# Kernel tuning notes

Hardware: AMD Instinct MI355X
Metric: run time of the kernel (lower is better)

## Reference

```python
import jax, jax.numpy as jnp
import numpy as np

B = 128      # graphs in batch
NPG = 128    # nodes per graph
F = 256      # num_node_features
D = 192      # d_model
NH = 8       # decoder heads
L = 4        # decoder layers
DFF = 512
DEG = 16     # avg degree
P = 32       # num_patch_nodes
EH = 96      # encoder_hidden = max(D//2, 48)
GH = 4       # GAT heads (layer 1)
EPS = 1e-5


def _init(key, shape, fan_in):
    return jax.random.normal(key, shape, jnp.float32) / np.sqrt(fan_in)


def setup_inputs() -> dict:
    key = jax.random.key(0)
    ks = jax.random.split(key, 40)
    N = B * NPG
    E = N * DEG
    off = jnp.repeat(jnp.arange(B, dtype=jnp.int32) * NPG, E // B)
    src = jax.random.randint(ks[1], (E,), 0, NPG, dtype=jnp.int32) + off
    dst = jax.random.randint(ks[2], (E,), 0, NPG, dtype=jnp.int32) + off
    inp = dict(
        subgraph_x=jax.random.normal(ks[0], (N, F), jnp.float32),
        subgraph_edge_index=jnp.stack([src, dst]),
        target_local_idx=jax.random.randint(ks[3], (B,), 0, NPG, dtype=jnp.int32),
        batch=jnp.repeat(jnp.arange(B, dtype=jnp.int32), NPG),
        num_patch_nodes=P,
    )
    # GAT encoder params (PyG GATConv layout: W [heads*out, in], att [heads, out])
    inp['gat1_w'] = _init(ks[4], (GH * EH, F), F)
    inp['gat1_att_src'] = _init(ks[5], (GH, EH), EH)
    inp['gat1_att_dst'] = _init(ks[6], (GH, EH), EH)
    inp['gat1_b'] = jnp.zeros((GH * EH,), jnp.float32)
    inp['gat2_w'] = _init(ks[7], (D, GH * EH), GH * EH)
    inp['gat2_att_src'] = _init(ks[8], (1, D), D)
    inp['gat2_att_dst'] = _init(ks[9], (1, D), D)
    inp['gat2_b'] = jnp.zeros((D,), jnp.float32)
    # TransformerDecoder layers (stacked over L)
    inp['sa_qkv_w'] = _init(ks[10], (L, 3 * D, D), D)
    inp['sa_qkv_b'] = jnp.zeros((L, 3 * D), jnp.float32)
    inp['sa_out_w'] = _init(ks[11], (L, D, D), D)
    inp['sa_out_b'] = jnp.zeros((L, D), jnp.float32)
    inp['ca_qkv_w'] = _init(ks[12], (L, 3 * D, D), D)
    inp['ca_qkv_b'] = jnp.zeros((L, 3 * D), jnp.float32)
    inp['ca_out_w'] = _init(ks[13], (L, D, D), D)
    inp['ca_out_b'] = jnp.zeros((L, D), jnp.float32)
    inp['ff1_w'] = _init(ks[14], (L, DFF, D), D)
    inp['ff1_b'] = jnp.zeros((L, DFF), jnp.float32)
    inp['ff2_w'] = _init(ks[15], (L, D, DFF), DFF)
    inp['ff2_b'] = jnp.zeros((L, D), jnp.float32)
    inp['ln_g'] = jnp.ones((L, 3, D), jnp.float32)
    inp['ln_b'] = jnp.zeros((L, 3, D), jnp.float32)
    # feature head
    inp['h1_w'] = _init(ks[16], (D, D), D)
    inp['h1_b'] = jnp.zeros((D,), jnp.float32)
    inp['h2_w'] = _init(ks[17], (F, D), D)
    inp['h2_b'] = jnp.zeros((F,), jnp.float32)
    return inp


def _gat(x, src, dst, W, a_src, a_dst, bias, heads, ch, concat):
    # PyG GATConv with add_self_loops=True, negative_slope=0.2, eval mode (no dropout)
    N = x.shape[0]
    xp = (x @ W.T).reshape(N, heads, ch)
    loop = jnp.arange(N, dtype=src.dtype)
    s = jnp.concatenate([src, loop])
    d = jnp.concatenate([dst, loop])
    al_s = (xp * a_src).sum(-1)  # [N, H]
    al_d = (xp * a_dst).sum(-1)
    e = jax.nn.leaky_relu(al_s[s] + al_d[d], 0.2)  # [E+N, H]
    emax = jax.ops.segment_max(e, d, num_segments=N)
    ex = jnp.exp(e - emax[d])
    den = jax.ops.segment_sum(ex, d, num_segments=N)
    coef = ex / (den[d] + 1e-16)
    out = jax.ops.segment_sum(xp[s] * coef[:, :, None], d, num_segments=N)  # [N,H,C]
    out = out.reshape(N, heads * ch) if concat else out.mean(1)
    return out + bias


def _ln(x, g, b):
    m = x.mean(-1, keepdims=True)
    v = ((x - m) ** 2).mean(-1, keepdims=True)
    return (x - m) / jnp.sqrt(v + EPS) * g + b


def _mha(q_in, kv_in, qkv_w, qkv_b, out_w, out_b, causal):
    b, sq, d = q_in.shape
    sk = kv_in.shape[1]
    dh = d // NH
    wq, wk, wv = jnp.split(qkv_w, 3, axis=0)
    bq, bk, bv = jnp.split(qkv_b, 3)
    q = (q_in @ wq.T + bq).reshape(b, sq, NH, dh).transpose(0, 2, 1, 3)
    k = (kv_in @ wk.T + bk).reshape(b, sk, NH, dh).transpose(0, 2, 1, 3)
    v = (kv_in @ wv.T + bv).reshape(b, sk, NH, dh).transpose(0, 2, 1, 3)
    sc = jnp.einsum('bhqd,bhkd->bhqk', q, k) / np.sqrt(dh).astype(np.float32)
    if causal:
        sc = jnp.where(jnp.tril(jnp.ones((sq, sk), bool)), sc, -1e30)
    a = jax.nn.softmax(sc, axis=-1)
    o = jnp.einsum('bhqk,bhkd->bhqd', a, v).transpose(0, 2, 1, 3).reshape(b, sq, d)
    return o @ out_w.T + out_b


def _pe(max_len, d):
    pos = jnp.arange(max_len, dtype=jnp.float32)[:, None]
    div = jnp.exp(jnp.arange(0, d, 2, dtype=jnp.float32) * (-np.log(10000.0) / d))
    pe = jnp.zeros((max_len, d), jnp.float32)
    return pe.at[:, 0::2].set(jnp.sin(pos * div)).at[:, 1::2].set(jnp.cos(pos * div))


def _forward(subgraph_x, gat1_w, gat1_att_src, gat1_att_dst, gat1_b,
             gat2_w, gat2_att_src, gat2_att_dst, gat2_b,
             sa_qkv_w, sa_qkv_b, sa_out_w, sa_out_b,
             ca_qkv_w, ca_qkv_b, ca_out_w, ca_out_b,
             ff1_w, ff1_b, ff2_w, ff2_b, ln_g, ln_b,
             h1_w, h1_b, h2_w, h2_b,
             subgraph_edge_index, target_local_idx, batch, num_patch_nodes):
    src, dst = subgraph_edge_index[0], subgraph_edge_index[1]
    h = jax.nn.elu(_gat(subgraph_x, src, dst, gat1_w, gat1_att_src, gat1_att_dst, gat1_b, GH, EH, True))
    mem = _gat(h, src, dst, gat2_w, gat2_att_src, gat2_att_dst, gat2_b, 1, D, False)
    bsz = target_local_idx.shape[0]
    mem_d = mem.reshape(bsz, -1, D)  # to_dense_batch: equal-sized, sorted graphs -> reshape, mask all-valid
    tgt = mem_d[jnp.arange(bsz), target_local_idx][:, None, :]  # [B,1,D]
    Pn = int(num_patch_nodes)
    pe = _pe(Pn + 1, D)
    feats = []
    adj = jnp.zeros((bsz, Pn + 1, Pn + 1), subgraph_x.dtype)
    for i in range(Pn):
        s = i + 1
        x = tgt + pe[None, :s]  # pos encoding (dropout is eval no-op)
        for l in range(L):
            x = _ln(x + _mha(x, x, sa_qkv_w[l], sa_qkv_b[l], sa_out_w[l], sa_out_b[l], True), ln_g[l, 0], ln_b[l, 0])
            x = _ln(x + _mha(x, mem_d, ca_qkv_w[l], ca_qkv_b[l], ca_out_w[l], ca_out_b[l], False), ln_g[l, 1], ln_b[l, 1])
            ff = jax.nn.gelu(x @ ff1_w[l].T + ff1_b[l], approximate=False) @ ff2_w[l].T + ff2_b[l]
            x = _ln(x + ff, ln_g[l, 2], ln_b[l, 2])
        last = x[:, -1]  # [B,D]
        feats.append(jax.nn.gelu(last @ h1_w.T + h1_b, approximate=False) @ h2_w.T + h2_b)
        cl = jnp.einsum('bsd,bd->bs', x, last)  # connection logits, len s
        adj = adj.at[:, i, Pn].set(cl[:, 0]).at[:, Pn, i].set(cl[:, 0])
        if i > 0:
            adj = adj.at[:, i, :i].set(cl[:, 1:i + 1]).at[:, :i, i].set(cl[:, 1:i + 1])
        tgt = jnp.concatenate([tgt, jax.lax.stop_gradient(last)[:, None]], axis=1)  # .detach() in torch
    adj = jnp.triu(adj, 1)
    adj = adj + jnp.swapaxes(adj, -1, -2)  # symmetric, zero diagonal
    return jnp.stack(feats, axis=1), adj


def reference(subgraph_x, subgraph_edge_index, target_local_idx, batch, num_patch_nodes,
              gat1_w, gat1_att_src, gat1_att_dst, gat1_b,
              gat2_w, gat2_att_src, gat2_att_dst, gat2_b,
              sa_qkv_w, sa_qkv_b, sa_out_w, sa_out_b,
              ca_qkv_w, ca_qkv_b, ca_out_w, ca_out_b,
              ff1_w, ff1_b, ff2_w, ff2_b, ln_g, ln_b,
              h1_w, h1_b, h2_w, h2_b):
    return _forward(subgraph_x, gat1_w, gat1_att_src, gat1_att_dst, gat1_b,
                    gat2_w, gat2_att_src, gat2_att_dst, gat2_b,
                    sa_qkv_w, sa_qkv_b, sa_out_w, sa_out_b,
                    ca_qkv_w, ca_qkv_b, ca_out_w, ca_out_b,
                    ff1_w, ff1_b, ff2_w, ff2_b, ln_g, ln_b,
                    h1_w, h1_b, h2_w, h2_b,
                    subgraph_edge_index, target_local_idx, batch, num_patch_nodes)
```

## Files before the change

kernel.cpp:

```cpp
#include <hip/hip_runtime.h>
#include <hip/hip_bf16.h>
#include <math.h>

#define DEV __device__ __forceinline__
typedef unsigned int u32;
typedef unsigned short u16;

constexpr int NNODES = 16384;
constexpr int NEDGE  = 262144;
constexpr int NEL    = NEDGE + NNODES;
constexpr int FIN    = 256;
constexpr int C1     = 384;
constexpr int DM     = 192;
constexpr int BZ     = 128;
constexpr int NPG_   = 128;
constexpr int LL     = 4;
constexpr int PP     = 32;
constexpr int SM     = 33;
constexpr int DFF_   = 512;

constexpr int PL4     = 52224;
constexpr int OFF4_QKV = 0;
constexpr int OFF4_SAO = 13824;
constexpr int OFF4_CAQ = 18432;
constexpr int OFF4_CAO = 23040;
constexpr int OFF4_FF1 = 27648;
constexpr int OFF4_FF2 = 39936;

constexpr size_t O_KVK = 0;
constexpr size_t O_VT  = 6291456;
constexpr size_t O_XP1 = 0;
constexpr size_t O_H   = 6291456;
constexpr size_t O_XP2 = 12582912;
constexpr size_t O_MEM = 15728640;
constexpr size_t O_WP  = 20545536;
constexpr size_t O_PE  = 21424128;
constexpr size_t O_AL1S= O_PE + 6336;
constexpr size_t O_AL1D= O_AL1S + 65536;
constexpr size_t O_AL2S= O_AL1D + 65536;
constexpr size_t O_AL2D= O_AL2S + 16384;
constexpr size_t O_CNT = O_AL2D + 16384;
constexpr size_t O_BASE= O_CNT + 16384;
constexpr size_t O_FILL= O_BASE + 16384;
constexpr size_t O_CSRC= O_FILL + 16384;
constexpr size_t O_LASTS=O_CSRC + 278528;

DEV float gelu_f(float v) { return 0.5f*v*(1.0f + erff(v*0.7071067811865475f)); }
DEV float bflo(u32 w) { return __uint_as_float(w << 16); }
DEV float bfhi(u32 w) { return __uint_as_float(w & 0xffff0000u); }
DEV float bfu(u16 u)  { return __uint_as_float(((u32)u) << 16); }
DEV u16 bf16u(float a) {
  __hip_bfloat16 h = __float2bfloat16(a);
  return *reinterpret_cast<u16*>(&h);
}
DEV u32 pk2(float a, float b) {
  return (u32)bf16u(a) | ((u32)bf16u(b) << 16);
}
DEV void fma8(float& a, uint4 w, float4 xa, float4 xb) {
  a = fmaf(bflo(w.x), xa.x, a); a = fmaf(bfhi(w.x), xa.y, a);
  a = fmaf(bflo(w.y), xa.z, a); a = fmaf(bfhi(w.y), xa.w, a);
  a = fmaf(bflo(w.z), xb.x, a); a = fmaf(bfhi(w.z), xb.y, a);
  a = fmaf(bflo(w.w), xb.z, a); a = fmaf(bfhi(w.w), xb.w, a);
}
template<int NU4, int STRIDE>
DEV float dotcol(const uint4* __restrict__ col, const float* __restrict__ xv) {
  const float4* x4 = (const float4*)xv;
  float a0 = 0, a1 = 0, a2 = 0, a3 = 0;
  #pragma unroll
  for (int q = 0; q < NU4; ++q) {
    uint4 w = col[(size_t)q*STRIDE];
    if ((q & 3) == 0) fma8(a0, w, x4[2*q], x4[2*q+1]);
    else if ((q & 3) == 1) fma8(a1, w, x4[2*q], x4[2*q+1]);
    else if ((q & 3) == 2) fma8(a2, w, x4[2*q], x4[2*q+1]);
    else fma8(a3, w, x4[2*q], x4[2*q+1]);
  }
  return (a0+a1)+(a2+a3);
}
template<int N> struct WB { uint4 w[N]; };
template<int N, int STRIDE>
DEV void wissue(WB<N>& r, const uint4* __restrict__ col) {
  #pragma unroll
  for (int q = 0; q < N; ++q) r.w[q] = col[(size_t)q*STRIDE];
}
template<int N>
DEV float wuse(const WB<N>& r, const float* __restrict__ xv) {
  const float4* x4 = (const float4*)xv;
  float a0 = 0, a1 = 0, a2 = 0, a3 = 0;
  #pragma unroll
  for (int q = 0; q < N; ++q) {
    float4 xa = x4[2*q], xb = x4[2*q+1];
    if ((q & 3) == 0) fma8(a0, r.w[q], xa, xb);
    else if ((q & 3) == 1) fma8(a1, r.w[q], xa, xb);
    else if ((q & 3) == 2) fma8(a2, r.w[q], xa, xb);
    else fma8(a3, r.w[q], xa, xb);
  }
  return (a0+a1)+(a2+a3);
}

__global__ void zero_kernel(float* adj, int* cnt, int* fill) {
  int i = blockIdx.x*256 + threadIdx.x;
  if (i < BZ*SM*SM) adj[i] = 0.f;
  if (i < NNODES) { cnt[i] = 0; fill[i] = 0; }
}

__global__ void pe_kernel(float* pe) {
  int idx = blockIdx.x*256 + threadIdx.x;
  if (idx >= SM*DM) return;
  int p = idx / DM, d = idx % DM;
  int i2 = d >> 1;
  float div = __expf((float)(2*i2) * (-9.210340371976184f / (float)DM));
  float a = (float)p * div;
  pe[idx] = (d & 1) ? cosf(a) : sinf(a);
}

__global__ void pack_kernel(const float* __restrict__ W, uint4* __restrict__ P, int N, int K) {
  int idx = blockIdx.x*256 + threadIdx.x;
  if (idx >= N*(K>>3)) return;
  int o = idx % N, kq = idx / N;
  const float* r = W + (size_t)o*K + 8*kq;
  uint4 u;
  u.x = pk2(r[0], r[1]); u.y = pk2(r[2], r[3]);
  u.z = pk2(r[4], r[5]); u.w = pk2(r[6], r[7]);
  P[idx] = u;
}

template<int BMODE, bool BF16OUT, bool GELU = false>
__global__ __launch_bounds__(256) void gemm_nt(const float* __restrict__ A,
    const float* __restrict__ W, const float* __restrict__ bias,
    float* __restrict__ Cf, __hip_bfloat16* __restrict__ Cb, int M, int N, int K)
{
  __shared__ float As[16][68];
  __shared__ float Ws[16][68];
  const int bm = blockIdx.y*64, bn = blockIdx.x*64;
  const int t = threadIdx.x, tx = t & 15, ty = t >> 4;
  float acc[4][4] = {};
  for (int k0 = 0; k0 < K; k0 += 16) {
    #pragma unroll
    for (int i = 0; i < 4; ++i) {
      int idx = t + i*256, kk = idx & 15, m = idx >> 4;
      As[kk][m] = A[(size_t)(bm+m)*K + k0+kk];
      Ws[kk][m] = W[(size_t)(bn+m)*K + k0+kk];
    }
    __syncthreads();
    #pragma unroll
    for (int kk = 0; kk < 16; ++kk) {
      const float4 a4 = *(const float4*)&As[kk][ty*4];
      const float4 b4 = *(const float4*)&Ws[kk][tx*4];
      const float av[4] = {a4.x,a4.y,a4.z,a4.w};
      const float bv[4] = {b4.x,b4.y,b4.z,b4.w};
      #pragma unroll
      for (int i = 0; i < 4; ++i)
        #pragma unroll
        for (int j = 0; j < 4; ++j)
          acc[i][j] = fmaf(av[i], bv[j], acc[i][j]);
    }
    __syncthreads();
  }
  #pragma unroll
  for (int i = 0; i < 4; ++i) {
    const int m = bm + ty*4 + i;
    #pragma unroll
    for (int j = 0; j < 4; ++j) {
      const int n = bn + tx*4 + j;
      float v = acc[i][j];
      if (BMODE == 1) v += bias[n];
      if (BMODE == 2) v += bias[m];
      if (GELU) v = gelu_f(v);
      if (BF16OUT) Cb[(size_t)m*N + n] = __float2bfloat16(v);
      else         Cf[(size_t)m*N + n] = v;
    }
  }
}

template<int HEADS, int CH>
__global__ void al_kernel(const float* __restrict__ xp, const float* __restrict__ asrc,
                          const float* __restrict__ adst, float* als, float* ald) {
  int idx = blockIdx.x*256 + threadIdx.x;
  if (idx >= NNODES*HEADS) return;
  int n = idx / HEADS, h = idx % HEADS;
  const float* row = xp + (size_t)n*(HEADS*CH) + h*CH;
  float s = 0, d = 0;
  for (int c = 0; c < CH; ++c) { float v = row[c]; s = fmaf(v, asrc[h*CH+c], s); d = fmaf(v, adst[h*CH+c], d); }
  als[idx] = s; ald[idx] = d;
}

__global__ void count_kernel(const int* __restrict__ dst, int* cnt) {
  int e = blockIdx.x*256 + threadIdx.x;
  if (e < NEDGE) atomicAdd(&cnt[dst[e]], 1);
}

__global__ __launch_bounds__(1024) void scan_kernel(const int* __restrict__ cnt, int* base) {
  __shared__ int tot[1024];
  int t = threadIdx.x;
  int local[16]; int s = 0;
  #pragma unroll
  for (int i = 0; i < 16; ++i) { int v = cnt[t*16+i] + 1; local[i] = s; s += v; }
  tot[t] = s; __syncthreads();
  if (t == 0) { int r = 0; for (int i = 0; i < 1024; ++i) { int v = tot[i]; tot[i] = r; r += v; } }
  __syncthreads();
  int off = tot[t];
  #pragma unroll
  for (int i = 0; i < 16; ++i) base[t*16+i] = off + local[i];
}

__global__ void scatter_kernel(const int* __restrict__ src, const int* __restrict__ dst,
                               const int* __restrict__ base, int* fill, int* csrc) {
  int e = blockIdx.x*256 + threadIdx.x;
  if (e < NEDGE) {
    int d = dst[e];
    int p = atomicAdd(&fill[d], 1);
    csrc[base[d] + p] = src[e];
  } else if (e < NEL) {
    int n = e - NEDGE;
    int p = atomicAdd(&fill[n], 1);
    csrc[base[n] + p] = n;
  }
}

template<int HEADS, int CH, bool ELU>
__global__ __launch_bounds__(128) void agg_kernel(const float* __restrict__ xp,
    const float* __restrict__ als, const float* __restrict__ ald,
    const int* __restrict__ cnt, const int* __restrict__ base, const int* __restrict__ csrc,
    const float* __restrict__ bias, float* __restrict__ out)
{
  constexpr int CO = HEADS*CH;
  constexpr int MAXD = 128;
  int n = blockIdx.x, t = threadIdx.x;
  int deg = cnt[n] + 1, st = base[n];
  if (deg > MAXD) deg = MAXD;
  __shared__ int   srcs[MAXD];
  __shared__ float ex[MAXD][HEADS];
  __shared__ float den[HEADS];
  for (int j = t; j < deg; j += 128) srcs[j] = csrc[st + j];
  __syncthreads();
  for (int idx = t; idx < deg*HEADS; idx += 128) {
    int j = idx / HEADS, h = idx % HEADS;
    float e = als[srcs[j]*HEADS + h] + ald[n*HEADS + h];
    ex[j][h] = (e > 0.f) ? e : 0.2f*e;
  }
  __syncthreads();
  if (t < HEADS) {
    float m = -1e30f;
    for (int j = 0; j < deg; ++j) m = fmaxf(m, ex[j][t]);
    float s = 0;
    for (int j = 0; j < deg; ++j) { float v = __expf(ex[j][t]-m); ex[j][t] = v; s += v; }
    den[t] = 1.0f/(s + 1e-16f);
  }
  __syncthreads();
  for (int c = t; c < CO; c += 128) {
    int h = c / CH;
    float acc = 0;
    for (int j = 0; j < deg; ++j) acc = fmaf(ex[j][h], xp[(size_t)srcs[j]*CO + c], acc);
    float v = acc*den[h] + bias[c];
    if (ELU) v = (v > 0.f) ? v : (__expf(v) - 1.0f);
    out[(size_t)n*CO + c] = v;
  }
}

__global__ void adj_kernel(const float* __restrict__ lastsG, float* __restrict__ adj) {
  int b = blockIdx.x, i = blockIdx.y, jj = threadIdx.x;
  if (jj > i) return;
  const float* li = lastsG + ((size_t)b*PP + i)*DM;
  const float* lj = lastsG + ((size_t)b*PP + jj)*DM;
  float a = 0.f;
  for (int d = 0; d < DM; ++d) a = fmaf(lj[d], li[d], a);
  if (jj == 0) {
    adj[((size_t)b*SM + i)*SM + 32] = a;
    adj[((size_t)b*SM + 32)*SM + i] = a;
  } else {
    adj[((size_t)b*SM + jj-1)*SM + i] = a;
    adj[((size_t)b*SM + i)*SM + jj-1] = a;
  }
}

__global__ __launch_bounds__(1024, 1) void decode_kernel(
    const float* __restrict__ mem, const u16* __restrict__ kvk, const u16* __restrict__ vT,
    const uint4* __restrict__ wp, const float* __restrict__ pe,
    const int* __restrict__ tgt_idx,
    const float* __restrict__ saqkvb, const float* __restrict__ saoutb,
    const float* __restrict__ caqkvb, const float* __restrict__ caoutb,
    const float* __restrict__ ff1b, const float* __restrict__ ff2b,
    const float* __restrict__ lng, const float* __restrict__ lnb,
    float* __restrict__ lastsG)
{
  const int b = blockIdx.x, t = threadIdx.x;
  const int wv = t >> 6, lane = t & 63;
  __shared__ u16   ksa16[4*33*194];
  __shared__ u16   vsa16[4*33*194];
  __shared__ __align__(16) float x[DM];
  __shared__ __align__(16) float qkv[DM];
  __shared__ __align__(16) float attno[DM];
  __shared__ __align__(16) float hid[DFF_];
  __shared__ float prob[33*9 + 7];
  __shared__ float cprob[128*9 + 2];
  __shared__ __align__(16) float psA[1152];
  __shared__ float painv[8], cainv[8], red[16];
  const float scl = 0.2041241452319315f;
  const float* tgt0 = mem + ((size_t)b*NPG_ + tgt_idx[b])*DM;
  const uint4* kvk4 = (const uint4*)kvk;

  const int qks = t / 576, qcol = t - qks*576;
  const int k4s = t >> 9,  o512 = t & 511;
  const int ks4 = (t < 768) ? t/192 : 0;
  const int o192 = t - ((t < 768) ? (t/192)*192 : 0);
  const int caj = t >> 3, cah = t & 7;

  WB<3> rCAK;

  auto ln_ps4 = [&](const float* g, const float* be) {
    float v = 0.f;
    if (t < DM) v = x[t] + ((psA[t]+psA[192+t]) + (psA[384+t]+psA[576+t]));
    float s = v, q = v*v;
    #pragma unroll
    for (int o = 32; o; o >>= 1) { s += __shfl_down(s, o, 64); q += __shfl_down(q, o, 64); }
    if (lane == 0 && wv < 3) { red[wv] = s; red[8+wv] = q; }
    __syncthreads();
    float S = red[0]+red[1]+red[2];
    float Q = red[8]+red[9]+red[10];
    float mu = S*(1.f/DM), var = Q*(1.f/DM) - mu*mu;
    float rstd = rsqrtf(var + 1e-5f);
    if (t < DM) x[t] = (v-mu)*rstd*g[t] + be[t];
    __syncthreads();
  };

  if (t < DM) x[t] = tgt0[t] + pe[t];
  __syncthreads();

  for (int i = 0; i < PP; ++i) {
    for (int l = 0; l < LL; ++l) {
      const uint4* WL = wp + (size_t)l*PL4;
      {
        psA[t] = (qks ? 0.f : saqkvb[l*576 + qcol]) + dotcol<12,576>(WL + OFF4_QKV + qks*12*576 + qcol, x + 96*qks);
        if (t < 128)
          psA[1024 + t] = dotcol<12,576>(WL + OFF4_QKV + 12*576 + 448 + t, x + 96);
      }
      wissue<3,1>(rCAK, kvk4 + ((size_t)l*NNODES + b*NPG_ + caj)*24 + cah*3);
      __syncthreads();
      if (t < 576) {
        float a = psA[t] + psA[576 + t];
        if (t < 192)      qkv[t] = a;
        else if (t < 384) ksa16[(l*33 + i)*194 + (t-192)] = bf16u(a);
        else              vsa16[(l*33 + i)*194 + (t-384)] = bf16u(a);
      }
      __syncthreads();
      if (wv < 8) {
        float s = -1e30f;
        if (lane <= i) {
          const u32* kr = (const u32*)ksa16 + ((size_t)l*33 + lane)*97 + wv*12;
          float a0 = 0, a1 = 0;
          #pragma unroll
          for (int c = 0; c < 12; c += 2) {
            u32 w0 = kr[c], w1 = kr[c+1];
            a0 = fmaf(bflo(w0), qkv[wv*24 + 2*c],   a0);
            a0 = fmaf(bfhi(w0), qkv[wv*24 + 2*c+1], a0);
            a1 = fmaf(bflo(w1), qkv[wv*24 + 2*c+2], a1);
            a1 = fmaf(bfhi(w1), qkv[wv*24 + 2*c+3], a1);
          }
          s = (a0+a1) * scl;
        }
        float m = s;
        #pragma unroll
        for (int o2 = 32; o2; o2 >>= 1) m = fmaxf(m, __shfl_xor(m, o2, 64));
        float e = (lane <= i) ? __expf(s - m) : 0.f;
        float sm = e;
        #pragma unroll
        for (int o2 = 32; o2; o2 >>= 1) sm += __shfl_xor(sm, o2, 64);
        if (lane <= i) prob[lane*9 + wv] = e;
        if (lane == 0) painv[wv] = 1.0f / sm;
      }
      __syncthreads();
      if (t < DM) {
        int hh = t / 24;
        const u16* vr = vsa16 + (size_t)l*33*194 + t;
        float a0 = 0, a1 = 0;
        for (int j = 0; j + 1 <= i; j += 2) {
          a0 = fmaf(prob[j*9 + hh],     bfu(vr[(size_t)j*194]),     a0);
          a1 = fmaf(prob[(j+1)*9 + hh], bfu(vr[(size_t)(j+1)*194]), a1);
        }
        if (!(i & 1)) a0 = fmaf(prob[i*9 + hh], bfu(vr[(size_t)i*194]), a0);
        attno[t] = (a0 + a1) * painv[hh];
      }
      __syncthreads();
      if (t < 768)
        psA[t] = (ks4 ? 0.f : saoutb[l*DM + o192]) + dotcol<6,192>(WL + OFF4_SAO + ks4*6*192 + o192, attno + 48*ks4);
      __syncthreads();
      ln_ps4(lng + (l*3+0)*DM, lnb + (l*3+0)*DM);
      if (t < 768)
        psA[t] = (ks4 ? 0.f : caqkvb[l*3*DM + o192]) + dotcol<6,192>(WL + OFF4_CAQ + ks4*6*192 + o192, x + 48*ks4);
      __syncthreads();
      {
        float4 qv4[6];
        const int cbase = cah*24;
        #pragma unroll
        for (int o2 = 0; o2 < 6; ++o2) {
          float4 v;
          int c0 = cbase + 4*o2;
          v.x = (psA[c0+0]+psA[192+c0+0]) + (psA[384+c0+0]+psA[576+c0+0]);
          v.y = (psA[c0+1]+psA[192+c0+1]) + (psA[384+c0+1]+psA[576+c0+1]);
          v.z = (psA[c0+2]+psA[192+c0+2]) + (psA[384+c0+2]+psA[576+c0+2]);
          v.w = (psA[c0+3]+psA[192+c0+3]) + (psA[384+c0+3]+psA[576+c0+3]);
          qv4[o2] = v;
        }
        cprob[caj*9 + cah] = scl * wuse<3>(rCAK, (const float*)qv4);
      }
      __syncthreads();
      if (wv < 8) {
        float s0 = cprob[lane*9 + wv], s1 = cprob[(lane+64)*9 + wv];
        float m = fmaxf(s0, s1);
        #pragma unroll
        for (int o2 = 32; o2; o2 >>= 1) m = fmaxf(m, __shfl_xor(m, o2, 64));
        float e0 = __expf(s0-m), e1 = __expf(s1-m);
        float sm = e0+e1;
        #pragma unroll
        for (int o2 = 32; o2; o2 >>= 1) sm += __shfl_xor(sm, o2, 64);
        cprob[lane*9 + wv] = e0; cprob[(lane+64)*9 + wv] = e1;
        if (lane == 0) cainv[wv] = 1.0f / sm;
      }
      __syncthreads();
      if (t < DM) {
        int hh = t / 24;
        const uint4* v4 = (const uint4*)(vT + ((size_t)l*DM + t)*NNODES + b*NPG_);
        float a0 = 0, a1 = 0;
        #pragma unroll
        for (int q = 0; q < 16; ++q) {
          uint4 w = v4[q];
          int j0 = q*8;
          a0 = fmaf(cprob[(j0+0)*9 + hh], bflo(w.x), a0);
          a1 = fmaf(cprob[(j0+1)*9 + hh], bfhi(w.x), a1);
          a0 = fmaf(cprob[(j0+2)*9 + hh], bflo(w.y), a0);
          a1 = fmaf(cprob[(j0+3)*9 + hh], bfhi(w.y), a1);
          a0 = fmaf(cprob[(j0+4)*9 + hh], bflo(w.z), a0);
          a1 = fmaf(cprob[(j0+5)*9 + hh], bfhi(w.z), a1);
          a0 = fmaf(cprob[(j0+6)*9 + hh], bflo(w.w), a0);
          a1 = fmaf(cprob[(j0+7)*9 + hh], bfhi(w.w), a1);
        }
        attno[t] = (a0 + a1) * cainv[hh];
      }
      __syncthreads();
      if (t < 768)
        psA[t] = (ks4 ? 0.f : caoutb[l*DM + o192]) + dotcol<6,192>(WL + OFF4_CAO + ks4*6*192 + o192, attno + 48*ks4);
      __syncthreads();
      ln_ps4(lng + (l*3+1)*DM, lnb + (l*3+1)*DM);
      psA[t] = (k4s ? 0.f : ff1b[l*DFF_ + o512]) + dotcol<12,512>(WL + OFF4_FF1 + k4s*12*512 + o512, x + 96*k4s);
      __syncthreads();
      if (t < DFF_) hid[t] = gelu_f(psA[t] + psA[512+t]);
      __syncthreads();
      if (t < 768)
        psA[t] = (ks4 ? 0.f : ff2b[l*DM + o192]) + dotcol<16,192>(WL + OFF4_FF2 + ks4*16*192 + o192, hid + 128*ks4);
      __syncthreads();
      ln_ps4(lng + (l*3+2)*DM, lnb + (l*3+2)*DM);
    }
    if (t < DM) {
      float xv = x[t];
      lastsG[((size_t)b*PP + i)*DM + t] = xv;
      if (i + 1 < PP) x[t] = xv + pe[(i+1)*DM + t];
    }
    __syncthreads();
  }
}

extern "C" void kernel_launch(void* const* d_in, const int* in_sizes, int n_in,
                              void* d_out, int out_size, void* d_ws, size_t ws_size,
                              hipStream_t stream) {
  (void)in_sizes; (void)n_in; (void)out_size; (void)ws_size;
  const float* x_in    = (const float*)d_in[0];
  const int*   ei      = (const int*)d_in[1];
  const int*   tgt_idx = (const int*)d_in[2];
  const float* gat1_w  = (const float*)d_in[5];
  const float* g1as    = (const float*)d_in[6];
  const float* g1ad    = (const float*)d_in[7];
  const float* g1b     = (const float*)d_in[8];
  const float* gat2_w  = (const float*)d_in[9];
  const float* g2as    = (const float*)d_in[10];
  const float* g2ad    = (const float*)d_in[11];
  const float* g2b     = (const float*)d_in[12];
  const float* saqkvw  = (const float*)d_in[13];
  const float* saqkvb  = (const float*)d_in[14];
  const float* saoutw  = (const float*)d_in[15];
  const float* saoutb  = (const float*)d_in[16];
  const float* caqkvw  = (const float*)d_in[17];
  const float* caqkvb  = (const float*)d_in[18];
  const float* caoutw  = (const float*)d_in[19];
  const float* caoutb  = (const float*)d_in[20];
  const float* ff1w    = (const float*)d_in[21];
  const float* ff1b    = (const float*)d_in[22];
  const float* ff2w    = (const float*)d_in[23];
  const float* ff2b    = (const float*)d_in[24];
  const float* lng     = (const float*)d_in[25];
  const float* lnb     = (const float*)d_in[26];
  const float* h1w     = (const float*)d_in[27];
  const float* h1b     = (const float*)d_in[28];
  const float* h2w     = (const float*)d_in[29];
  const float* h2b     = (const float*)d_in[30];

  float* ws  = (float*)d_ws;
  float* out = (float*)d_out;
  float* adj = out + (size_t)BZ*PP*256;

  const int* src = ei;
  const int* dst = ei + NEDGE;

  int* cnt  = (int*)(ws + O_CNT);
  int* base = (int*)(ws + O_BASE);
  int* fill = (int*)(ws + O_FILL);
  int* csrc = (int*)(ws + O_CSRC);
  float* lastsG = ws + O_LASTS;
  float* hidG   = ws + O_XP2;

  hipLaunchKernelGGL(zero_kernel, dim3(545), dim3(256), 0, stream, adj, cnt, fill);

  hipLaunchKernelGGL((gemm_nt<0,false>), dim3(C1/64, NNODES/64), dim3(256), 0, stream,
                     x_in, gat1_w, (const float*)nullptr, ws + O_XP1, (__hip_bfloat16*)nullptr,
                     NNODES, C1, FIN);
  hipLaunchKernelGGL((al_kernel<4,96>), dim3(NNODES*4/256), dim3(256), 0, stream,
                     ws+O_XP1, g1as, g1ad, ws+O_AL1S, ws+O_AL1D);
  hipLaunchKernelGGL(count_kernel, dim3(NEDGE/256), dim3(256), 0, stream, dst, cnt);
  hipLaunchKernelGGL(scan_kernel, dim3(1), dim3(1024), 0, stream, cnt, base);
  hipLaunchKernelGGL(scatter_kernel, dim3(NEL/256), dim3(256), 0, stream, src, dst, base, fill, csrc);
  hipLaunchKernelGGL((agg_kernel<4,96,true>), dim3(NNODES), dim3(128), 0, stream,
                     ws+O_XP1, ws+O_AL1S, ws+O_AL1D, cnt, base, csrc, g1b, ws+O_H);

  hipLaunchKernelGGL((gemm_nt<0,false>), dim3(DM/64, NNODES/64), dim3(256), 0, stream,
                     ws+O_H, gat2_w, (const float*)nullptr, ws+O_XP2, (__hip_bfloat16*)nullptr,
                     NNODES, DM, C1);
  hipLaunchKernelGGL((al_kernel<1,192>), dim3(NNODES/256), dim3(256), 0, stream,
                     ws+O_XP2, g2as, g2ad, ws+O_AL2S, ws+O_AL2D);
  hipLaunchKernelGGL((agg_kernel<1,192,false>), dim3(NNODES), dim3(128), 0, stream,
                     ws+O_XP2, ws+O_AL2S, ws+O_AL2D, cnt, base, csrc, g2b, ws+O_MEM);

  uint4* wp = (uint4*)(ws + O_WP);
  auto PK = [&](const float* Wsrc, int off_u4, int N, int K) {
    hipLaunchKernelGGL(pack_kernel, dim3((N*(K/8)+255)/256), dim3(256), 0, stream,
                       Wsrc, wp + off_u4, N, K);
  };
  for (int l = 0; l < LL; ++l) {
    PK(saqkvw + (size_t)l*110592, l*PL4 + OFF4_QKV, 576, 192);
    PK(saoutw + (size_t)l*36864,  l*PL4 + OFF4_SAO, 192, 192);
    PK(caqkvw + (size_t)l*110592, l*PL4 + OFF4_CAQ, 192, 192);
    PK(caoutw + (size_t)l*36864,  l*PL4 + OFF4_CAO, 192, 192);
    PK(ff1w   + (size_t)l*98304,  l*PL4 + OFF4_FF1, 512, 192);
    PK(ff2w   + (size_t)l*98304,  l*PL4 + OFF4_FF2, 192, 512);
  }

  hipLaunchKernelGGL(pe_kernel, dim3((SM*DM+255)/256), dim3(256), 0, stream, ws+O_PE);

  __hip_bfloat16* kvk = (__hip_bfloat16*)(ws + O_KVK);
  __hip_bfloat16* vT  = (__hip_bfloat16*)(ws + O_VT);
  for (int l = 0; l < LL; ++l) {
    hipLaunchKernelGGL((gemm_nt<1,true>), dim3(DM/64, NNODES/64), dim3(256), 0, stream,
                       ws+O_MEM, caqkvw + (size_t)l*110592 + (size_t)192*192,
                       caqkvb + l*576 + 192, (float*)nullptr,
                       kvk + (size_t)l*NNODES*DM, NNODES, DM, DM);
    hipLaunchKernelGGL((gemm_nt<2,true>), dim3(NNODES/64, DM/64), dim3(256), 0, stream,
                       caqkvw + (size_t)l*110592 + (size_t)2*192*192, ws+O_MEM,
                       caqkvb + l*576 + 384, (float*)nullptr,
                       vT + (size_t)l*DM*NNODES, DM, NNODES, DM);
  }

  hipLaunchKernelGGL(decode_kernel, dim3(BZ), dim3(1024), 0, stream,
                     ws+O_MEM, (const u16*)kvk, (const u16*)vT, wp, ws+O_PE, tgt_idx,
                     saqkvb, saoutb, caqkvb, caoutb, ff1b, ff2b, lng, lnb,
                     lastsG);

  hipLaunchKernelGGL((gemm_nt<1,false,true>), dim3(DM/64, (BZ*PP)/64), dim3(256), 0, stream,
                     lastsG, h1w, h1b, hidG, (__hip_bfloat16*)nullptr,
                     BZ*PP, DM, DM);
  hipLaunchKernelGGL((gemm_nt<1,false,false>), dim3(256/64, (BZ*PP)/64), dim3(256), 0, stream,
                     hidG, h2w, h2b, out, (__hip_bfloat16*)nullptr,
                     BZ*PP, 256, DM);
  hipLaunchKernelGGL(adj_kernel, dim3(BZ, PP), dim3(64), 0, stream, lastsG, adj);
}
```

Measured before the change: 3.783 ms.

## Drop split-K partial sums in decoder matvecs and fuse attention stages

Each decoder matvec now computes its full dot product in one thread per output column instead of splitting K across thread groups and reducing partial sums through a shared psA buffer. The self- and cross-attention weighted-value sums move into the softmax warps, so the softmax result is used directly from registers. Together these remove several __syncthreads barriers and shared-memory round trips per layer step. The cost is that fewer threads are active in each matvec, with longer serial dot products (for example 64 uint4 chunks for FF2), which lowers parallelism within the block.

```diff
diff --git a/kernel.cpp b/kernel.cpp
--- a/kernel.cpp
+++ b/kernel.cpp
@@ -293,35 +293,13 @@
   __shared__ __align__(16) float hid[DFF_];
   __shared__ float prob[33*9 + 7];
   __shared__ float cprob[128*9 + 2];
-  __shared__ __align__(16) float psA[1152];
-  __shared__ float painv[8], cainv[8], red[16];
+  __shared__ float red[16];
   const float scl = 0.2041241452319315f;
   const float* tgt0 = mem + ((size_t)b*NPG_ + tgt_idx[b])*DM;
   const uint4* kvk4 = (const uint4*)kvk;
-
-  const int qks = t / 576, qcol = t - qks*576;
-  const int k4s = t >> 9,  o512 = t & 511;
-  const int ks4 = (t < 768) ? t/192 : 0;
-  const int o192 = t - ((t < 768) ? (t/192)*192 : 0);
   const int caj = t >> 3, cah = t & 7;
 
   WB<3> rCAK;
-
-  auto ln_ps4 = [&](const float* g, const float* be) {
-    float v = 0.f;
-    if (t < DM) v = x[t] + ((psA[t]+psA[192+t]) + (psA[384+t]+psA[576+t]));
-    float s = v, q = v*v;
-    #pragma unroll
-    for (int o = 32; o; o >>= 1) { s += __shfl_down(s, o, 64); q += __shfl_down(q, o, 64); }
-    if (lane == 0 && wv < 3) { red[wv] = s; red[8+wv] = q; }
-    __syncthreads();
-    float S = red[0]+red[1]+red[2];
-    float Q = red[8]+red[9]+red[10];
-    float mu = S*(1.f/DM), var = Q*(1.f/DM) - mu*mu;
-    float rstd = rsqrtf(var + 1e-5f);
-    if (t < DM) x[t] = (v-mu)*rstd*g[t] + be[t];
-    __syncthreads();
-  };
 
   if (t < DM) x[t] = tgt0[t] + pe[t];
   __syncthreads();
@@ -329,19 +307,13 @@
   for (int i = 0; i < PP; ++i) {
     for (int l = 0; l < LL; ++l) {
       const uint4* WL = wp + (size_t)l*PL4;
-      {
-        psA[t] = (qks ? 0.f : saqkvb[l*576 + qcol]) + dotcol<12,576>(WL + OFF4_QKV + qks*12*576 + qcol, x + 96*qks);
-        if (t < 128)
-          psA[1024 + t] = dotcol<12,576>(WL + OFF4_QKV + 12*576 + 448 + t, x + 96);
-      }
-      wissue<3,1>(rCAK, kvk4 + ((size_t)l*NNODES + b*NPG_ + caj)*24 + cah*3);
-      __syncthreads();
       if (t < 576) {
-        float a = psA[t] + psA[576 + t];
+        float a = saqkvb[l*576 + t] + dotcol<24,576>(WL + OFF4_QKV + t, x);
         if (t < 192)      qkv[t] = a;
         else if (t < 384) ksa16[(l*33 + i)*194 + (t-192)] = bf16u(a);
         else              vsa16[(l*33 + i)*194 + (t-384)] = bf16u(a);
       }
+      wissue<3,1>(rCAK, kvk4 + ((size_t)l*NNODES + b*NPG_ + caj)*24 + cah*3);
       __syncthreads();
       if (wv < 8) {
         float s = -1e30f;
@@ -366,43 +338,42 @@
         #pragma unroll
         for (int o2 = 32; o2; o2 >>= 1) sm += __shfl_xor(sm, o2, 64);
         if (lane <= i) prob[lane*9 + wv] = e;
-        if (lane == 0) painv[wv] = 1.0f / sm;
-      }
-      __syncthreads();
-      if (t < DM) {
-        int hh = t / 24;
-        const u16* vr = vsa16 + (size_t)l*33*194 + t;
-        float a0 = 0, a1 = 0;
-        for (int j = 0; j + 1 <= i; j += 2) {
-          a0 = fmaf(prob[j*9 + hh],     bfu(vr[(size_t)j*194]),     a0);
-          a1 = fmaf(prob[(j+1)*9 + hh], bfu(vr[(size_t)(j+1)*194]), a1);
+        float pinv = 1.0f / sm;
+        if (lane < 24) {
+          const u16* vr = vsa16 + (size_t)l*33*194 + wv*24 + lane;
+          float a0 = 0, a1 = 0;
+          for (int j = 0; j + 1 <= i; j += 2) {
+            a0 = fmaf(prob[j*9 + wv],     bfu(vr[(size_t)j*194]),     a0);
+            a1 = fmaf(prob[(j+1)*9 + wv], bfu(vr[(size_t)(j+1)*194]), a1);
+          }
+          if (!(i & 1)) a0 = fmaf(prob[i*9 + wv], bfu(vr[(size_t)i*194]), a0);
+          attno[wv*24 + lane] = (a0 + a1) * pinv;
         }
-        if (!(i & 1)) a0 = fmaf(prob[i*9 + hh], bfu(vr[(size_t)i*194]), a0);
-        attno[t] = (a0 + a1) * painv[hh];
-      }
-      __syncthreads();
-      if (t < 768)
-        psA[t] = (ks4 ? 0.f : saoutb[l*DM + o192]) + dotcol<6,192>(WL + OFF4_SAO + ks4*6*192 + o192, attno + 48*ks4);
-      __syncthreads();
-      ln_ps4(lng + (l*3+0)*DM, lnb + (l*3+0)*DM);
-      if (t < 768)
-        psA[t] = (ks4 ? 0.f : caqkvb[l*3*DM + o192]) + dotcol<6,192>(WL + OFF4_CAQ + ks4*6*192 + o192, x + 48*ks4);
-      __syncthreads();
+      }
+      __syncthreads();
+      float v1 = 0.f;
       {
-        float4 qv4[6];
-        const int cbase = cah*24;
-        #pragma unroll
-        for (int o2 = 0; o2 < 6; ++o2) {
-          float4 v;
-          int c0 = cbase + 4*o2;
-          v.x = (psA[c0+0]+psA[192+c0+0]) + (psA[384+c0+0]+psA[576+c0+0]);
-          v.y = (psA[c0+1]+psA[192+c0+1]) + (psA[384+c0+1]+psA[576+c0+1]);
-          v.z = (psA[c0+2]+psA[192+c0+2]) + (psA[384+c0+2]+psA[576+c0+2]);
-          v.w = (psA[c0+3]+psA[192+c0+3]) + (psA[384+c0+3]+psA[576+c0+3]);
-          qv4[o2] = v;
+        if (t < DM) {
+          float a = saoutb[l*DM + t] + dotcol<24,192>(WL + OFF4_SAO + t, attno);
+          v1 = x[t] + a;
         }
-        cprob[caj*9 + cah] = scl * wuse<3>(rCAK, (const float*)qv4);
-      }
+        float s = v1, q = v1*v1;
+        #pragma unroll
+        for (int o = 32; o; o >>= 1) { s += __shfl_down(s, o, 64); q += __shfl_down(q, o, 64); }
+        if (lane == 0 && wv < 3) { red[wv] = s; red[8+wv] = q; }
+      }
+      __syncthreads();
+      {
+        float S = red[0]+red[1]+red[2], Q = red[8]+red[9]+red[10];
+        float mu = S*(1.f/DM), var = Q*(1.f/DM) - mu*mu;
+        float rstd = rsqrtf(var + 1e-5f);
+        if (t < DM) x[t] = (v1-mu)*rstd*lng[(l*3+0)*DM + t] + lnb[(l*3+0)*DM + t];
+      }
+      __syncthreads();
+      if (t < DM)
+        qkv[t] = caqkvb[l*3*DM + t] + dotcol<24,192>(WL + OFF4_CAQ + t, x);
+      __syncthreads();
+      cprob[caj*9 + cah] = scl * wuse<3>(rCAK, qkv + cah*24);
       __syncthreads();
       if (wv < 8) {
         float s0 = cprob[lane*9 + wv], s1 = cprob[(lane+64)*9 + wv];
@@ -414,41 +385,69 @@
         #pragma unroll
         for (int o2 = 32; o2; o2 >>= 1) sm += __shfl_xor(sm, o2, 64);
         cprob[lane*9 + wv] = e0; cprob[(lane+64)*9 + wv] = e1;
-        if (lane == 0) cainv[wv] = 1.0f / sm;
-      }
-      __syncthreads();
-      if (t < DM) {
-        int hh = t / 24;
-        const uint4* v4 = (const uint4*)(vT + ((size_t)l*DM + t)*NNODES + b*NPG_);
-        float a0 = 0, a1 = 0;
-        #pragma unroll
-        for (int q = 0; q < 16; ++q) {
-          uint4 w = v4[q];
-          int j0 = q*8;
-          a0 = fmaf(cprob[(j0+0)*9 + hh], bflo(w.x), a0);
-          a1 = fmaf(cprob[(j0+1)*9 + hh], bfhi(w.x), a1);
-          a0 = fmaf(cprob[(j0+2)*9 + hh], bflo(w.y), a0);
-          a1 = fmaf(cprob[(j0+3)*9 + hh], bfhi(w.y), a1);
-          a0 = fmaf(cprob[(j0+4)*9 + hh], bflo(w.z), a0);
-          a1 = fmaf(cprob[(j0+5)*9 + hh], bfhi(w.z), a1);
-          a0 = fmaf(cprob[(j0+6)*9 + hh], bflo(w.w), a0);
-          a1 = fmaf(cprob[(j0+7)*9 + hh], bfhi(w.w), a1);
+        float cinv = 1.0f / sm;
+        if (lane < 24) {
+          const int d = wv*24 + lane;
+          const uint4* v4 = (const uint4*)(vT + ((size_t)l*DM + d)*NNODES + b*NPG_);
+          float a0 = 0, a1 = 0;
+          #pragma unroll
+          for (int q = 0; q < 16; ++q) {
+            uint4 w = v4[q];
+            int j0 = q*8;
+            a0 = fmaf(cprob[(j0+0)*9 + wv], bflo(w.x), a0);
+            a1 = fmaf(cprob[(j0+1)*9 + wv], bfhi(w.x), a1);
+            a0 = fmaf(cprob[(j0+2)*9 + wv], bflo(w.y), a0);
+            a1 = fmaf(cprob[(j0+3)*9 + wv], bfhi(w.y), a1);
+            a0 = fmaf(cprob[(j0+4)*9 + wv], bflo(w.z), a0);
+            a1 = fmaf(cprob[(j0+5)*9 + wv], bfhi(w.z), a1);
+            a0 = fmaf(cprob[(j0+6)*9 + wv], bflo(w.w), a0);
+            a1 = fmaf(cprob[(j0+7)*9 + wv], bfhi(w.w), a1);
+          }
+          attno[d] = (a0 + a1) * cinv;
         }
-        attno[t] = (a0 + a1) * cainv[hh];
-      }
-      __syncthreads();
-      if (t < 768)
-        psA[t] = (ks4 ? 0.f : caoutb[l*DM + o192]) + dotcol<6,192>(WL + OFF4_CAO + ks4*6*192 + o192, attno + 48*ks4);
-      __syncthreads();
-      ln_ps4(lng + (l*3+1)*DM, lnb + (l*3+1)*DM);
-      psA[t] = (k4s ? 0.f : ff1b[l*DFF_ + o512]) + dotcol<12,512>(WL + OFF4_FF1 + k4s*12*512 + o512, x + 96*k4s);
-      __syncthreads();
-      if (t < DFF_) hid[t] = gelu_f(psA[t] + psA[512+t]);
-      __syncthreads();
-      if (t < 768)
-        psA[t] = (ks4 ? 0.f : ff2b[l*DM + o192]) + dotcol<16,192>(WL + OFF4_FF2 + ks4*16*192 + o192, hid + 128*ks4);
-      __syncthreads();
-      ln_ps4(lng + (l*3+2)*DM, lnb + (l*3+2)*DM);
+      }
+      __syncthreads();
+      float v2 = 0.f;
+      {
+        if (t < DM) {
+          float a = caoutb[l*DM + t] + dotcol<24,192>(WL + OFF4_CAO + t, attno);
+          v2 = x[t] + a;
+        }
+        float s = v2, q = v2*v2;
+        #pragma unroll
+        for (int o = 32; o; o >>= 1) { s += __shfl_down(s, o, 64); q += __shfl_down(q, o, 64); }
+        if (lane == 0 && wv < 3) { red[wv] = s; red[8+wv] = q; }
+      }
+      __syncthreads();
+      {
+        float S = red[0]+red[1]+red[2], Q = red[8]+red[9]+red[10];
+        float mu = S*(1.f/DM), var = Q*(1.f/DM) - mu*mu;
+        float rstd = rsqrtf(var + 1e-5f);
+        if (t < DM) x[t] = (v2-mu)*rstd*lng[(l*3+1)*DM + t] + lnb[(l*3+1)*DM + t];
+      }
+      __syncthreads();
+      if (t < DFF_)
+        hid[t] = gelu_f(ff1b[l*DFF_ + t] + dotcol<24,512>(WL + OFF4_FF1 + t, x));
+      __syncthreads();
+      float v3 = 0.f;
+      {
+        if (t < DM) {
+          float a = ff2b[l*DM + t] + dotcol<64,192>(WL + OFF4_FF2 + t, hid);
+          v3 = x[t] + a;
+        }
+        float s = v3, q = v3*v3;
+        #pragma unroll
+        for (int o = 32; o; o >>= 1) { s += __shfl_down(s, o, 64); q += __shfl_down(q, o, 64); }
+        if (lane == 0 && wv < 3) { red[wv] = s; red[8+wv] = q; }
+      }
+      __syncthreads();
+      {
+        float S = red[0]+red[1]+red[2], Q = red[8]+red[9]+red[10];
+        float mu = S*(1.f/DM), var = Q*(1.f/DM) - mu*mu;
+        float rstd = rsqrtf(var + 1e-5f);
+        if (t < DM) x[t] = (v3-mu)*rstd*lng[(l*3+2)*DM + t] + lnb[(l*3+2)*DM + t];
+      }
+      __syncthreads();
     }
     if (t < DM) {
       float xv = x[t];
```

Result: slower. 5.943 ms (+57.1%).
